# Kernel tuning notes

Measured on AMD Instinct MI355X. Metric: run time of the kernel, lower is better.

Reference implementation:

```python
import jax, jax.numpy as jnp
import numpy as np

N = 50000      # nodes
IN = 128       # in_channels
H = 2          # heads
C = 64         # hidden_channels (per head)
E = 800000     # edges (before self-loops)
OUT = 40       # out_channels
BN_EPS = 1e-5
NEG_SLOPE = 0.2  # PyG GATConv default


def _bn(x, g, b):
    # BatchNorm1d forward with batch statistics (training-mode math, biased var)
    mu = jnp.mean(x, axis=0)
    v = jnp.var(x, axis=0)
    return (x - mu) * jax.lax.rsqrt(v + BN_EPS) * g + b


def _gat_conv(x, src, dst, W, a_src, a_dst, bias, concat):
    n = x.shape[0]
    h = (x @ W).reshape(n, H, C)                      # [N,H,C] per-head projection
    al_s = jnp.einsum('nhc,hc->nh', h, a_src)         # [N,H]
    al_d = jnp.einsum('nhc,hc->nh', h, a_dst)
    e = jax.nn.leaky_relu(al_s[src] + al_d[dst], NEG_SLOPE)  # [E,H]
    # segment softmax over edges sharing the same destination
    m = jax.ops.segment_max(e, dst, num_segments=n)
    ex = jnp.exp(e - m[dst])
    s = jax.ops.segment_sum(ex, dst, num_segments=n)
    alpha = ex / s[dst]                               # [E,H]
    out = jax.ops.segment_sum(h[src] * alpha[..., None], dst, num_segments=n)  # [N,H,C]
    out = out.reshape(n, H * C) if concat else out.mean(axis=1)
    return out + bias


def setup_inputs() -> dict:
    key = jax.random.key(0)
    ks = jax.random.split(key, 16)
    g = lambda k, shp, scale=1.0: jax.random.normal(k, shp, dtype=jnp.float32) * scale
    x = g(ks[0], (N, IN))
    edge_index = jax.random.randint(ks[1], (2, E), 0, N, dtype=jnp.int32)
    s = 1.0 / np.sqrt(IN)
    s2 = 1.0 / np.sqrt(H * C)
    return {
        'x': x,
        'edge_index': edge_index,
        'bn0_g': jnp.ones((IN,), jnp.float32), 'bn0_b': jnp.zeros((IN,), jnp.float32),
        'W1': g(ks[2], (IN, H * C), s), 'a1_src': g(ks[3], (H, C), s), 'a1_dst': g(ks[4], (H, C), s),
        'b1': jnp.zeros((H * C,), jnp.float32),
        'bn1_g': jnp.ones((H * C,), jnp.float32), 'bn1_b': jnp.zeros((H * C,), jnp.float32),
        'W2': g(ks[5], (H * C, H * C), s2), 'a2_src': g(ks[6], (H, C), s2), 'a2_dst': g(ks[7], (H, C), s2),
        'b2': jnp.zeros((C,), jnp.float32),
        'bn2_g': jnp.ones((C,), jnp.float32), 'bn2_b': jnp.zeros((C,), jnp.float32),
        'Wf': g(ks[8], (C, OUT), 1.0 / np.sqrt(C)), 'bf': jnp.zeros((OUT,), jnp.float32),
    }


def reference(x, edge_index, bn0_g, bn0_b, W1, a1_src, a1_dst, b1, bn1_g, bn1_b,
              W2, a2_src, a2_dst, b2, bn2_g, bn2_b, Wf, bf):
    n = x.shape[0]
    loop = jnp.arange(n, dtype=edge_index.dtype)
    src = jnp.concatenate([edge_index[0], loop])  # add self-loops (PyG default)
    dst = jnp.concatenate([edge_index[1], loop])
    h = _bn(x, bn0_g, bn0_b)
    # layer 1: concat heads
    h = _gat_conv(h, src, dst, W1, a1_src, a1_dst, b1, concat=True)
    h = jax.nn.elu(_bn(h, bn1_g, bn1_b))
    # (dropout is identity in eval mode)
    # layer 2: average heads
    h = _gat_conv(h, src, dst, W2, a2_src, a2_dst, b2, concat=False)
    h = jax.nn.elu(_bn(h, bn2_g, bn2_b))
    return h @ Wf + bf
```

## Files before the change

kernel.cpp:

```cpp
#include <hip/hip_runtime.h>
#include <hip/hip_fp16.h>


#define NEG_SLOPE 0.2f
#define BN_EPS 1e-5f

typedef short bf16x8 __attribute__((ext_vector_type(8)));
typedef float f32x4 __attribute__((ext_vector_type(4)));

static __device__ __forceinline__ unsigned short f2bf(float f) {
    union { float f; unsigned u; } v; v.f = f;
    unsigned r = v.u + 0x7FFF + ((v.u >> 16) & 1);
    return (unsigned short)(r >> 16);
}
static __device__ __forceinline__ float2 bf2x2(unsigned v) {
    union { unsigned u; float f; } a, b;
    a.u = v << 16; b.u = v & 0xffff0000u;
    return make_float2(a.f, b.f);
}
static __device__ __forceinline__ float halfsel(unsigned p, int head) {
    __half2 h = *(__half2*)&p;
    return head ? __high2float(h) : __low2float(h);
}

template <int C>
static __device__ __forceinline__ void d_bnstat(const float* __restrict__ x, int M,
                                                int rowsPerBlock, float* __restrict__ sums,
                                                int b) {
    constexpr int TPR = C / 4;
    constexpr int RS  = 256 / TPR;
    __shared__ float red[4][2 * C];
    const int t = threadIdx.x;
    const int cg = t % TPR, rg = t / TPR, w = t >> 6, lane = t & 63;
    int r0 = b * rowsPerBlock + rg;
    int r1 = min(M, b * rowsPerBlock + rowsPerBlock);
    float4 s = make_float4(0, 0, 0, 0), q = make_float4(0, 0, 0, 0);
    #pragma unroll 4
    for (int r = r0; r < r1; r += RS) {
        float4 v = *(const float4*)&x[(size_t)r * C + cg * 4];
        s.x += v.x; s.y += v.y; s.z += v.z; s.w += v.w;
        q.x += v.x * v.x; q.y += v.y * v.y; q.z += v.z * v.z; q.w += v.w * v.w;
    }
    #pragma unroll
    for (int off = TPR; off < 64; off <<= 1) {
        s.x += __shfl_xor(s.x, off); s.y += __shfl_xor(s.y, off);
        s.z += __shfl_xor(s.z, off); s.w += __shfl_xor(s.w, off);
        q.x += __shfl_xor(q.x, off); q.y += __shfl_xor(q.y, off);
        q.z += __shfl_xor(q.z, off); q.w += __shfl_xor(q.w, off);
    }
    if (lane < TPR) {
        *(float4*)&red[w][cg * 4] = s;
        *(float4*)&red[w][C + cg * 4] = q;
    }
    __syncthreads();
    for (int idx = t; idx < 2 * C; idx += 256) {
        float tot = red[0][idx] + red[1][idx] + red[2][idx] + red[3][idx];
        atomicAdd(&sums[idx], tot);
    }
}

template <int C>
__global__ __launch_bounds__(256) void k_bnstat2(const float* __restrict__ x, int M,
                                                 int rowsPerBlock, float* __restrict__ sums) {
    d_bnstat<C>(x, M, rowsPerBlock, sums, blockIdx.x);
}

__global__ __launch_bounds__(256) void k_prep(
    const int* __restrict__ ei, int E, int rgrid,
    const float* __restrict__ x, int M, int bgrid,
    const float* __restrict__ W1, const float* __restrict__ W2,
    int* __restrict__ cnt, unsigned short* __restrict__ rank,
    float* __restrict__ sums,
    unsigned short* __restrict__ wt1, unsigned short* __restrict__ wt2) {
    int b = blockIdx.x;
    if (b < rgrid) {
        int i = b * 256 + threadIdx.x;
        if (i < E) {
            int d = ei[E + i];
            int p = b & 7;
            rank[i] = (unsigned short)atomicAdd(&cnt[(size_t)p * M + d], 1);
        }
    } else if (b < rgrid + bgrid) {
        d_bnstat<128>(x, M, 256, sums, b - rgrid);
    } else {
        int idx = (b - rgrid - bgrid) * 256 + threadIdx.x;
        if (idx < 128 * 128) {
            int n = idx >> 7, k = idx & 127;
            wt1[idx] = f2bf(W1[k * 128 + n]);
            wt2[idx] = f2bf(W2[k * 128 + n]);
        }
    }
}

__global__ __launch_bounds__(1024) void k_part(const int* __restrict__ cnt, int Nn,
                                               int* __restrict__ part) {
    __shared__ int ws[16];
    int t = threadIdx.x, lane = t & 63, w = t >> 6;
    int i = blockIdx.x * 1024 + t;
    int v = 0;
    if (i < Nn) {
        #pragma unroll
        for (int p = 0; p < 8; p++) v += cnt[(size_t)p * Nn + i];
        v += 1;
    }
    #pragma unroll
    for (int off = 32; off; off >>= 1) v += __shfl_xor(v, off);
    if (lane == 0) ws[w] = v;
    __syncthreads();
    if (t < 16) {
        int s = ws[t];
        #pragma unroll
        for (int off = 8; off; off >>= 1) s += __shfl_xor(s, off);
        if (t == 0) part[blockIdx.x] = s;
    }
}

__global__ __launch_bounds__(1024) void k_scan2(const int* __restrict__ cnt, int Nn, int nb,
                                                const int* __restrict__ part,
                                                int* __restrict__ rowptr,
                                                unsigned short* __restrict__ pofs) {
    __shared__ int wsum[16];
    __shared__ int s_base, s_total;
    int t = threadIdx.x, lane = t & 63, w = t >> 6;
    int b = blockIdx.x;
    if (w == 0) {
        int base = 0, total = 0;
        for (int ch = 0; ch < nb; ch += 64) {
            int j = ch + lane;
            int v = (j < nb) ? part[j] : 0;
            total += v;
            base += (j < b) ? v : 0;
        }
        #pragma unroll
        for (int off = 32; off; off >>= 1) {
            base += __shfl_xor(base, off);
            total += __shfl_xor(total, off);
        }
        if (lane == 0) { s_base = base; s_total = total; }
    }
    int i = b * 1024 + t;
    int v = 0;
    if (i < Nn) {
        int run = 0;
        #pragma unroll
        for (int p = 0; p < 8; p++) {
            pofs[(size_t)p * Nn + i] = (unsigned short)run;
            run += cnt[(size_t)p * Nn + i];
        }
        v = run + 1;
    }
    int x = v;
    #pragma unroll
    for (int off = 1; off < 64; off <<= 1) {
        int y = __shfl_up(x, off);
        if (lane >= off) x += y;
    }
    if (lane == 63) wsum[w] = x;
    __syncthreads();
    if (w == 0) {
        int val = (lane < 16) ? wsum[lane] : 0;
        int xs = val;
        #pragma unroll
        for (int off = 1; off < 16; off <<= 1) {
            int y = __shfl_up(xs, off);
            if (lane >= off) xs += y;
        }
        if (lane < 16) wsum[lane] = xs - val;
    }
    __syncthreads();
    if (i < Nn) rowptr[i] = s_base + wsum[w] + (x - v);
    if (b == nb - 1 && t == 0) rowptr[Nn] = s_total;
}

static __device__ __forceinline__ void d_fill(int b, const int* __restrict__ ei,
                                              const unsigned short* __restrict__ rank,
                                              const unsigned short* __restrict__ pofs,
                                              const int* __restrict__ rowptr, int E, int Nn,
                                              unsigned short* __restrict__ ssrc) {
    int i = b * 256 + threadIdx.x;
    if (i < E) {
        int s = ei[i], d = ei[E + i];
        int p = (i >> 8) & 7;
        int r = (int)pofs[(size_t)p * Nn + d] + (int)rank[i];
        ssrc[rowptr[d] + 1 + r] = (unsigned short)s;
    } else if (i < E + Nn) {
        int d = i - E;
        ssrc[rowptr[d]] = (unsigned short)d;
    }
}

static __device__ __forceinline__ void d_mfma(
    int blk, const float* __restrict__ A, const unsigned short* __restrict__ wt,
    const float* __restrict__ sums, const float* __restrict__ bng, const float* __restrict__ bnb,
    int elu, const float* __restrict__ asrc, const float* __restrict__ adst, int M,
    unsigned short* __restrict__ hb, float* __restrict__ als, float* __restrict__ ald) {
    __shared__ unsigned short As[64 * 136];
    __shared__ unsigned short Bs[128 * 136];
    __shared__ __align__(16) float stl[256];
    const int t = threadIdx.x;
    const int w = t >> 6, lane = t & 63;
    const int c = lane & 15, q = lane >> 4;
    const int row0 = blk * 64;

    if (t < 128) {
        float mu = sums[t] / (float)M;
        float var = sums[128 + t] / (float)M - mu * mu;
        float s = bng[t] * rsqrtf(var + BN_EPS);
        stl[t] = s;
        stl[128 + t] = bnb[t] - mu * s;
    }
    __syncthreads();

    #pragma unroll
    for (int i = 0; i < 8; i++) {
        int idx = t + i * 256;
        int r = idx >> 5, ch4 = idx & 31;
        int gr = row0 + r;
        float4 v = make_float4(0, 0, 0, 0);
        if (gr < M) {
            v = *(const float4*)&A[(size_t)gr * 128 + ch4 * 4];
            float4 sc = *(const float4*)&stl[ch4 * 4];
            float4 sh = *(const float4*)&stl[128 + ch4 * 4];
            v.x = v.x * sc.x + sh.x; v.y = v.y * sc.y + sh.y;
            v.z = v.z * sc.z + sh.z; v.w = v.w * sc.w + sh.w;
            if (elu) {
                v.x = v.x > 0.f ? v.x : expm1f(v.x);
                v.y = v.y > 0.f ? v.y : expm1f(v.y);
                v.z = v.z > 0.f ? v.z : expm1f(v.z);
                v.w = v.w > 0.f ? v.w : expm1f(v.w);
            }
        }
        unsigned p0 = ((unsigned)f2bf(v.y) << 16) | f2bf(v.x);
        unsigned p1 = ((unsigned)f2bf(v.w) << 16) | f2bf(v.z);
        *(uint2*)&As[r * 136 + ch4 * 4] = make_uint2(p0, p1);
    }
    #pragma unroll
    for (int i = 0; i < 8; i++) {
        int idx = t + i * 256;
        int r = idx >> 4, ch = idx & 15;
        *(uint4*)&Bs[r * 136 + ch * 8] = *(const uint4*)&wt[(size_t)r * 128 + ch * 8];
    }
    __syncthreads();

    f32x4 acc[8] = {};
    #pragma unroll
    for (int ks = 0; ks < 4; ks++) {
        bf16x8 a = *(bf16x8*)&As[(w * 16 + c) * 136 + (ks * 4 + q) * 8];
        #pragma unroll
        for (int tl = 0; tl < 8; tl++) {
            bf16x8 b = *(bf16x8*)&Bs[(tl * 16 + c) * 136 + (ks * 4 + q) * 8];
            acc[tl] = __builtin_amdgcn_mfma_f32_16x16x32_bf16(a, b, acc[tl], 0, 0, 0);
        }
    }

    #pragma unroll
    for (int reg = 0; reg < 4; reg++) {
        int grow = row0 + w * 16 + q * 4 + reg;
        if (grow < M) {
            #pragma unroll
            for (int tl = 0; tl < 8; tl++)
                hb[(size_t)grow * 128 + tl * 16 + c] = f2bf(acc[tl][reg]);
        }
    }

    float as_[8], ad_[8];
    #pragma unroll
    for (int tl = 0; tl < 8; tl++) { as_[tl] = asrc[tl * 16 + c]; ad_[tl] = adst[tl * 16 + c]; }
    #pragma unroll
    for (int reg = 0; reg < 4; reg++) {
        float s0 = 0.f, s1 = 0.f, d0 = 0.f, d1 = 0.f;
        #pragma unroll
        for (int tl = 0; tl < 4; tl++) { s0 += acc[tl][reg] * as_[tl]; d0 += acc[tl][reg] * ad_[tl]; }
        #pragma unroll
        for (int tl = 4; tl < 8; tl++) { s1 += acc[tl][reg] * as_[tl]; d1 += acc[tl][reg] * ad_[tl]; }
        #pragma unroll
        for (int off = 1; off < 16; off <<= 1) {
            s0 += __shfl_xor(s0, off); s1 += __shfl_xor(s1, off);
            d0 += __shfl_xor(d0, off); d1 += __shfl_xor(d1, off);
        }
        int grow = row0 + w * 16 + q * 4 + reg;
        if (c == 0 && grow < M) {
            *(float2*)&als[(size_t)grow * 2] = make_float2(s0, s1);
            *(float2*)&ald[(size_t)grow * 2] = make_float2(d0, d1);
        }
    }
}

__global__ __launch_bounds__(256) void k_mfma(
    const float* __restrict__ A, const unsigned short* __restrict__ wt,
    const float* __restrict__ sums, const float* __restrict__ bng, const float* __restrict__ bnb,
    int elu, const float* __restrict__ asrc, const float* __restrict__ adst, int M,
    unsigned short* __restrict__ hb, float* __restrict__ als, float* __restrict__ ald) {
    d_mfma(blockIdx.x, A, wt, sums, bng, bnb, elu, asrc, adst, M, hb, als, ald);
}

__global__ __launch_bounds__(256) void k_fill_mfma(
    const float* __restrict__ A, const unsigned short* __restrict__ wt,
    const float* __restrict__ sums, const float* __restrict__ bng, const float* __restrict__ bnb,
    const float* __restrict__ asrc, const float* __restrict__ adst, int M, int ggrid,
    unsigned short* __restrict__ hb, float* __restrict__ als, float* __restrict__ ald,
    const int* __restrict__ ei, const unsigned short* __restrict__ rank,
    const unsigned short* __restrict__ pofs,
    const int* __restrict__ rowptr, int E, int Nn, unsigned short* __restrict__ ssrc) {
    if (blockIdx.x < ggrid)
        d_mfma(blockIdx.x, A, wt, sums, bng, bnb, 0, asrc, adst, M, hb, als, ald);
    else
        d_fill(blockIdx.x - ggrid, ei, rank, pofs, rowptr, E, Nn, ssrc);
}

static __device__ __forceinline__ void acc8(float* acc, uint4 v, float a) {
    float2 p;
    p = bf2x2(v.x); acc[0] += a * p.x; acc[1] += a * p.y;
    p = bf2x2(v.y); acc[2] += a * p.x; acc[3] += a * p.y;
    p = bf2x2(v.z); acc[4] += a * p.x; acc[5] += a * p.y;
    p = bf2x2(v.w); acc[6] += a * p.x; acc[7] += a * p.y;
}

template <int MEAN>
static __device__ __forceinline__ void attnagg(
    const int* __restrict__ rowptr, const unsigned short* __restrict__ ssrc,
    const float* __restrict__ als, const float* __restrict__ ald,
    float* __restrict__ alpha, const unsigned short* __restrict__ hb,
    const float* __restrict__ bias, int Nn, float* __restrict__ out) {
    int gw = (blockIdx.x * blockDim.x + threadIdx.x) >> 6;
    if (gw >= Nn) return;
    int lane = threadIdx.x & 63;
    int sub = lane >> 4, c = lane & 15, head = c >> 3;
    int beg = rowptr[gw], end = rowptr[gw + 1];
    int deg = end - beg;
    float2 dv = *(const float2*)&ald[(size_t)gw * 2];
    float acc[8] = {};

    if (deg <= 64) {
        bool on = lane < deg;
        int eidx = beg + (on ? lane : 0);
        int sreg = (int)ssrc[eidx];
        float2 av = *(const float2*)&als[(size_t)sreg * 2];
        float v0 = av.x + dv.x; v0 = v0 > 0.f ? v0 : NEG_SLOPE * v0;
        float v1 = av.y + dv.y; v1 = v1 > 0.f ? v1 : NEG_SLOPE * v1;
        float p0 = on ? __expf(v0) : 0.f;
        float p1 = on ? __expf(v1) : 0.f;
        float t0 = p0, t1 = p1;
        #pragma unroll
        for (int off = 32; off; off >>= 1) {
            t0 += __shfl_xor(t0, off);
            t1 += __shfl_xor(t1, off);
        }
        __half2 hpk = __floats2half2_rn(p0 / t0, p1 / t1);
        unsigned pk = *(unsigned*)&hpk;

        int nit = (deg + 3) >> 2;
        int it = 0;
        for (; it + 4 <= nit; it += 4) {
            int s_[4]; float a_[4];
            #pragma unroll
            for (int u = 0; u < 4; u++) {
                int jj = (it + u) * 4 + sub;
                int ls = jj & 63;
                s_[u] = __shfl(sreg, ls);
                unsigned pw = (unsigned)__shfl(pk, ls);
                a_[u] = (jj < deg) ? halfsel(pw, head) : 0.f;
            }
            #pragma unroll
            for (int u = 0; u < 4; u++) {
                uint4 v = *(const uint4*)&hb[(size_t)s_[u] * 128 + c * 8];
                acc8(acc, v, a_[u]);
            }
        }
        for (; it < nit; it += 2) {
            const bool two = (it + 1) < nit;
            int s_[2]; float a_[2];
            #pragma unroll
            for (int u = 0; u < 2; u++) {
                if (u == 0 || two) {
                    int jj = (it + u) * 4 + sub;
                    int ls = jj & 63;
                    s_[u] = __shfl(sreg, ls);
                    unsigned pw = (unsigned)__shfl(pk, ls);
                    a_[u] = (jj < deg) ? halfsel(pw, head) : 0.f;
                }
            }
            #pragma unroll
            for (int u = 0; u < 2; u++) {
                if (u == 0 || two) {
                    uint4 v = *(const uint4*)&hb[(size_t)s_[u] * 128 + c * 8];
                    acc8(acc, v, a_[u]);
                }
            }
        }
    } else {
        float d0 = dv.x, d1 = dv.y;
        float m0 = -1e30f, m1 = -1e30f;
        for (int e = beg + lane; e < end; e += 64) {
            int s = (int)ssrc[e];
            float v0 = als[s * 2] + d0;     v0 = v0 > 0.f ? v0 : NEG_SLOPE * v0;
            float v1 = als[s * 2 + 1] + d1; v1 = v1 > 0.f ? v1 : NEG_SLOPE * v1;
            m0 = fmaxf(m0, v0); m1 = fmaxf(m1, v1);
        }
        #pragma unroll
        for (int off = 32; off; off >>= 1) {
            m0 = fmaxf(m0, __shfl_xor(m0, off));
            m1 = fmaxf(m1, __shfl_xor(m1, off));
        }
        float t0 = 0.f, t1 = 0.f;
        for (int e = beg + lane; e < end; e += 64) {
            int s = (int)ssrc[e];
            float v0 = als[s * 2] + d0;     v0 = v0 > 0.f ? v0 : NEG_SLOPE * v0;
            float v1 = als[s * 2 + 1] + d1; v1 = v1 > 0.f ? v1 : NEG_SLOPE * v1;
            float p0 = __expf(v0 - m0), p1 = __expf(v1 - m1);
            alpha[e * 2] = p0; alpha[e * 2 + 1] = p1;
            t0 += p0; t1 += p1;
        }
        #pragma unroll
        for (int off = 32; off; off >>= 1) {
            t0 += __shfl_xor(t0, off);
            t1 += __shfl_xor(t1, off);
        }
        float i0 = 1.f / t0, i1 = 1.f / t1;
        for (int e = beg + sub; e < end; e += 4) {
            int s = (int)ssrc[e];
            float a = (head ? alpha[(size_t)e * 2 + 1] * i1 : alpha[(size_t)e * 2] * i0);
            uint4 v = *(const uint4*)&hb[(size_t)s * 128 + c * 8];
            acc8(acc, v, a);
        }
    }

    #pragma unroll
    for (int j2 = 0; j2 < 8; j2++) {
        acc[j2] += __shfl_xor(acc[j2], 16);
        acc[j2] += __shfl_xor(acc[j2], 32);
        if (MEAN) acc[j2] += __shfl_xor(acc[j2], 8);
    }
    if (MEAN) {
        if (sub == 0 && c < 8) {
            float4 b0 = *(const float4*)&bias[c * 8];
            float4 b1 = *(const float4*)&bias[c * 8 + 4];
            float4 o0 = make_float4(0.5f * acc[0] + b0.x, 0.5f * acc[1] + b0.y, 0.5f * acc[2] + b0.z, 0.5f * acc[3] + b0.w);
            float4 o1 = make_float4(0.5f * acc[4] + b1.x, 0.5f * acc[5] + b1.y, 0.5f * acc[6] + b1.z, 0.5f * acc[7] + b1.w);
            *(float4*)&out[(size_t)gw * 64 + c * 8] = o0;
            *(float4*)&out[(size_t)gw * 64 + c * 8 + 4] = o1;
        }
    } else {
        if (sub == 0) {
            float4 b0 = *(const float4*)&bias[c * 8];
            float4 b1 = *(const float4*)&bias[c * 8 + 4];
            float4 o0 = make_float4(acc[0] + b0.x, acc[1] + b0.y, acc[2] + b0.z, acc[3] + b0.w);
            float4 o1 = make_float4(acc[4] + b1.x, acc[5] + b1.y, acc[6] + b1.z, acc[7] + b1.w);
            *(float4*)&out[(size_t)gw * 128 + c * 8] = o0;
            *(float4*)&out[(size_t)gw * 128 + c * 8 + 4] = o1;
        }
    }
}

__global__ __launch_bounds__(256) void k_attnagg1(const int* __restrict__ rowptr, const unsigned short* __restrict__ ssrc,
                                                  const float* __restrict__ als, const float* __restrict__ ald,
                                                  float* __restrict__ alpha, const unsigned short* __restrict__ hb,
                                                  const float* __restrict__ bias, int Nn, float* __restrict__ out) {
    attnagg<0>(rowptr, ssrc, als, ald, alpha, hb, bias, Nn, out);
}

__global__ __launch_bounds__(256) void k_attnagg2(const int* __restrict__ rowptr, const unsigned short* __restrict__ ssrc,
                                                  const float* __restrict__ als, const float* __restrict__ ald,
                                                  float* __restrict__ alpha, const unsigned short* __restrict__ hb,
                                                  const float* __restrict__ bias, int Nn, float* __restrict__ out) {
    attnagg<1>(rowptr, ssrc, als, ald, alpha, hb, bias, Nn, out);
}

__global__ __launch_bounds__(128) void k_gemmf(const float* __restrict__ A, const float* __restrict__ Wf,
                                               const float* __restrict__ bf,
                                               const float* __restrict__ sums, const float* __restrict__ bng,
                                               const float* __restrict__ bnb,
                                               int M, float* __restrict__ out) {
    __shared__ float As[128 * 65];
    __shared__ float Bs[64 * 40];
    __shared__ float stl[128];
    int t = threadIdx.x;
    int row0 = blockIdx.x * 128;
    if (t < 64) {
        float mu = sums[t] / (float)M;
        float var = sums[64 + t] / (float)M - mu * mu;
        float s = bng[t] * rsqrtf(var + BN_EPS);
        stl[t] = s;
        stl[64 + t] = bnb[t] - mu * s;
    }
    __syncthreads();
    for (int i = t; i < 64 * 40; i += 128) Bs[i] = Wf[i];
    for (int i = t; i < 128 * 64; i += 128) {
        int r = i >> 6, k = i & 63;
        int gr = row0 + r;
        float v = 0.f;
        if (gr < M) {
            v = A[(size_t)gr * 64 + k] * stl[k] + stl[64 + k];
            v = v > 0.f ? v : expm1f(v);
        }
        As[r * 65 + k] = v;
    }
    __syncthreads();
    int cg = t & 3, rg = t >> 2;
    float acc[4][10] = {};
    for (int k = 0; k < 64; k++) {
        float b[10];
        #pragma unroll
        for (int j = 0; j < 10; j++) b[j] = Bs[k * 40 + cg * 10 + j];
        #pragma unroll
        for (int r = 0; r < 4; r++) {
            float a = As[(rg * 4 + r) * 65 + k];
            #pragma unroll
            for (int j = 0; j < 10; j++) acc[r][j] += a * b[j];
        }
    }
    for (int r = 0; r < 4; r++) {
        int gr = row0 + rg * 4 + r;
        if (gr < M) {
            #pragma unroll
            for (int j = 0; j < 10; j++) out[(size_t)gr * 40 + cg * 10 + j] = acc[r][j] + bf[cg * 10 + j];
        }
    }
}

extern "C" void kernel_launch(void* const* d_in, const int* in_sizes, int n_in,
                              void* d_out, int out_size, void* d_ws, size_t ws_size,
                              hipStream_t stream) {
    const float* x     = (const float*)d_in[0];
    const int*   ei    = (const int*)d_in[1];
    const float* bn0_g = (const float*)d_in[2];
    const float* bn0_b = (const float*)d_in[3];
    const float* W1    = (const float*)d_in[4];
    const float* a1s   = (const float*)d_in[5];
    const float* a1d   = (const float*)d_in[6];
    const float* b1    = (const float*)d_in[7];
    const float* bn1_g = (const float*)d_in[8];
    const float* bn1_b = (const float*)d_in[9];
    const float* W2    = (const float*)d_in[10];
    const float* a2s   = (const float*)d_in[11];
    const float* a2d   = (const float*)d_in[12];
    const float* b2    = (const float*)d_in[13];
    const float* bn2_g = (const float*)d_in[14];
    const float* bn2_b = (const float*)d_in[15];
    const float* Wf    = (const float*)d_in[16];
    const float* bf    = (const float*)d_in[17];
    float* out = (float*)d_out;

    const int N  = in_sizes[0] / 128;
    const int E  = in_sizes[1] / 2;
    const int ET = E + N;

    char* ws = (char*)d_ws;
    size_t off = 0;
    auto alloc = [&](size_t bytes) -> char* {
        char* p = ws + off;
        off = (off + bytes + 255) & ~(size_t)255;
        return p;
    };
    int*   cnt    = (int*)alloc((size_t)8 * N * 4);
    float* sums   = (float*)alloc(640 * 4);
    const size_t zlen = off;
    int*   rowptr = (int*)alloc((size_t)(N + 1) * 4);
    unsigned short* ssrc = (unsigned short*)alloc((size_t)ET * 2);
    unsigned short* rank = (unsigned short*)alloc((size_t)E * 2);
    unsigned short* pofs = (unsigned short*)alloc((size_t)8 * N * 2);
    float* abuf   = (float*)alloc((size_t)N * 128 * 4);
    unsigned short* hb  = (unsigned short*)alloc((size_t)N * 128 * 2);
    unsigned short* wt1 = (unsigned short*)alloc((size_t)128 * 128 * 2);
    unsigned short* wt2 = (unsigned short*)alloc((size_t)128 * 128 * 2);
    float* alpha  = (float*)alloc((size_t)ET * 2 * 4);
    float* als    = (float*)alloc((size_t)N * 2 * 4);
    float* ald    = (float*)alloc((size_t)N * 2 * 4);
    int*   part   = (int*)alloc(1024 * 4);

    const int tb = 256;
    const int rgrid = (E + tb - 1) / tb;
    const int bgrid = (N + 255) / 256;
    const int fgrid = (ET + tb - 1) / tb;
    const int wgrid = ((size_t)N * 64 + tb - 1) / tb;
    const int ggrid = (N + 63) / 64;
    const int nscan = (N + 1023) / 1024;

    hipMemsetAsync(ws, 0, zlen, stream);

    k_prep<<<rgrid + bgrid + 64, tb, 0, stream>>>(ei, E, rgrid, x, N, bgrid, W1, W2,
                                                  cnt, rank, sums, wt1, wt2);
    k_part<<<nscan, 1024, 0, stream>>>(cnt, N, part);
    k_scan2<<<nscan, 1024, 0, stream>>>(cnt, N, nscan, part, rowptr, pofs);

    k_fill_mfma<<<ggrid + fgrid, tb, 0, stream>>>(x, wt1, sums, bn0_g, bn0_b,
                                                  a1s, a1d, N, ggrid, hb, als, ald,
                                                  ei, rank, pofs, rowptr, E, N, ssrc);
    k_attnagg1<<<wgrid, tb, 0, stream>>>(rowptr, ssrc, als, ald, alpha, hb, b1, N, abuf);

    k_bnstat2<128><<<bgrid, 256, 0, stream>>>(abuf, N, 256, sums + 256);

    k_mfma<<<ggrid, tb, 0, stream>>>(abuf, wt2, sums + 256, bn1_g, bn1_b, 1, a2s, a2d, N, hb, als, ald);
    k_attnagg2<<<wgrid, tb, 0, stream>>>(rowptr, ssrc, als, ald, alpha, hb, b2, N, abuf);

    k_bnstat2<64><<<bgrid, 256, 0, stream>>>(abuf, N, 256, sums + 512);

    k_gemmf<<<(N + 127) / 128, 128, 0, stream>>>(abuf, Wf, bf, sums + 512, bn2_g, bn2_b, N, out);
}
```

Baseline: 308.6 us.

## Count edge ranks with LDS histograms per node-range and edge-segment

Replaces the global-atomic degree counting, which used 8 partitioned int counters, with blocks that each own one edge segment of 32768 edges and one eighth of the node range. Each block histograms its destinations in shared memory, records ranks, and writes ushort counts per segment. The scan kernel turns these counts into per-segment offsets in place, so the separate pofs buffer and the zero-memset of cnt go away. In exchange, every block rereads its whole edge segment, so edge reads grow eightfold, and the scan kernels now loop over about 25 segments instead of 8.

```diff
diff --git a/kernel.cpp b/kernel.cpp
--- a/kernel.cpp
+++ b/kernel.cpp
@@ -66,24 +66,39 @@
 }
 
 __global__ __launch_bounds__(256) void k_prep(
-    const int* __restrict__ ei, int E, int rgrid,
+    const int* __restrict__ ei, int E, int S, int NR,
     const float* __restrict__ x, int M, int bgrid,
     const float* __restrict__ W1, const float* __restrict__ W2,
-    int* __restrict__ cnt, unsigned short* __restrict__ rank,
+    unsigned short* __restrict__ cnt, unsigned short* __restrict__ rank,
     float* __restrict__ sums,
     unsigned short* __restrict__ wt1, unsigned short* __restrict__ wt2) {
     int b = blockIdx.x;
-    if (b < rgrid) {
-        int i = b * 256 + threadIdx.x;
-        if (i < E) {
-            int d = ei[E + i];
-            int p = b & 7;
-            rank[i] = (unsigned short)atomicAdd(&cnt[(size_t)p * M + d], 1);
-        }
-    } else if (b < rgrid + bgrid) {
-        d_bnstat<128>(x, M, 256, sums, b - rgrid);
+    int CG = 8 * S;
+    if (b < CG) {
+        __shared__ unsigned lcnt[8192];
+        const int t = threadIdx.x;
+        const int r = b & 7, s = b >> 3;
+        const unsigned lo = (unsigned)(r * NR);
+        for (int j = t; j < NR; j += 256) lcnt[j] = 0;
+        __syncthreads();
+        int i1 = min(E, (s + 1) << 15);
+        for (int i = (s << 15) + t; i < i1; i += 256) {
+            unsigned d = (unsigned)ei[E + i];
+            unsigned rel = d - lo;
+            if (rel < (unsigned)NR) {
+                unsigned old = atomicAdd(&lcnt[rel], 1u);
+                rank[i] = (unsigned short)old;
+            }
+        }
+        __syncthreads();
+        for (int j = t; j < NR; j += 256) {
+            int node = (int)lo + j;
+            if (node < M) cnt[(size_t)s * M + node] = (unsigned short)lcnt[j];
+        }
+    } else if (b < CG + bgrid) {
+        d_bnstat<128>(x, M, 256, sums, b - CG);
     } else {
-        int idx = (b - rgrid - bgrid) * 256 + threadIdx.x;
+        int idx = (b - CG - bgrid) * 256 + threadIdx.x;
         if (idx < 128 * 128) {
             int n = idx >> 7, k = idx & 127;
             wt1[idx] = f2bf(W1[k * 128 + n]);
@@ -92,15 +107,14 @@
     }
 }
 
-__global__ __launch_bounds__(1024) void k_part(const int* __restrict__ cnt, int Nn,
-                                               int* __restrict__ part) {
+__global__ __launch_bounds__(1024) void k_part(const unsigned short* __restrict__ cnt,
+                                               int Nn, int S, int* __restrict__ part) {
     __shared__ int ws[16];
     int t = threadIdx.x, lane = t & 63, w = t >> 6;
     int i = blockIdx.x * 1024 + t;
     int v = 0;
     if (i < Nn) {
-        #pragma unroll
-        for (int p = 0; p < 8; p++) v += cnt[(size_t)p * Nn + i];
+        for (int s = 0; s < S; s++) v += (int)cnt[(size_t)s * Nn + i];
         v += 1;
     }
     #pragma unroll
@@ -115,10 +129,10 @@
     }
 }
 
-__global__ __launch_bounds__(1024) void k_scan2(const int* __restrict__ cnt, int Nn, int nb,
+__global__ __launch_bounds__(1024) void k_scan2(unsigned short* __restrict__ cnt,
+                                                int Nn, int S, int nb,
                                                 const int* __restrict__ part,
-                                                int* __restrict__ rowptr,
-                                                unsigned short* __restrict__ pofs) {
+                                                int* __restrict__ rowptr) {
     __shared__ int wsum[16];
     __shared__ int s_base, s_total;
     int t = threadIdx.x, lane = t & 63, w = t >> 6;
@@ -142,10 +156,10 @@
     int v = 0;
     if (i < Nn) {
         int run = 0;
-        #pragma unroll
-        for (int p = 0; p < 8; p++) {
-            pofs[(size_t)p * Nn + i] = (unsigned short)run;
-            run += cnt[(size_t)p * Nn + i];
+        for (int s = 0; s < S; s++) {
+            int cv = (int)cnt[(size_t)s * Nn + i];
+            cnt[(size_t)s * Nn + i] = (unsigned short)run;
+            run += cv;
         }
         v = run + 1;
     }
@@ -180,9 +194,9 @@
     int i = b * 256 + threadIdx.x;
     if (i < E) {
         int s = ei[i], d = ei[E + i];
-        int p = (i >> 8) & 7;
-        int r = (int)pofs[(size_t)p * Nn + d] + (int)rank[i];
-        ssrc[rowptr[d] + 1 + r] = (unsigned short)s;
+        int p = i >> 15;
+        int rk = (int)pofs[(size_t)p * Nn + d] + (int)rank[i];
+        ssrc[rowptr[d] + 1 + rk] = (unsigned short)s;
     } else if (i < E + Nn) {
         int d = i - E;
         ssrc[rowptr[d]] = (unsigned short)d;
@@ -544,6 +558,8 @@
     const int N  = in_sizes[0] / 128;
     const int E  = in_sizes[1] / 2;
     const int ET = E + N;
+    const int S  = (E + 32767) >> 15;
+    const int NR = (N + 7) / 8;
 
     char* ws = (char*)d_ws;
     size_t off = 0;
@@ -552,13 +568,12 @@
         off = (off + bytes + 255) & ~(size_t)255;
         return p;
     };
-    int*   cnt    = (int*)alloc((size_t)8 * N * 4);
     float* sums   = (float*)alloc(640 * 4);
     const size_t zlen = off;
+    unsigned short* cnt = (unsigned short*)alloc((size_t)S * N * 2);
     int*   rowptr = (int*)alloc((size_t)(N + 1) * 4);
     unsigned short* ssrc = (unsigned short*)alloc((size_t)ET * 2);
     unsigned short* rank = (unsigned short*)alloc((size_t)E * 2);
-    unsigned short* pofs = (unsigned short*)alloc((size_t)8 * N * 2);
     float* abuf   = (float*)alloc((size_t)N * 128 * 4);
     unsigned short* hb  = (unsigned short*)alloc((size_t)N * 128 * 2);
     unsigned short* wt1 = (unsigned short*)alloc((size_t)128 * 128 * 2);
@@ -569,7 +584,7 @@
     int*   part   = (int*)alloc(1024 * 4);
 
     const int tb = 256;
-    const int rgrid = (E + tb - 1) / tb;
+    const int CG = 8 * S;
     const int bgrid = (N + 255) / 256;
     const int fgrid = (ET + tb - 1) / tb;
     const int wgrid = ((size_t)N * 64 + tb - 1) / tb;
@@ -578,14 +593,14 @@
 
     hipMemsetAsync(ws, 0, zlen, stream);
 
-    k_prep<<<rgrid + bgrid + 64, tb, 0, stream>>>(ei, E, rgrid, x, N, bgrid, W1, W2,
-                                                  cnt, rank, sums, wt1, wt2);
-    k_part<<<nscan, 1024, 0, stream>>>(cnt, N, part);
-    k_scan2<<<nscan, 1024, 0, stream>>>(cnt, N, nscan, part, rowptr, pofs);
+    k_prep<<<CG + bgrid + 64, tb, 0, stream>>>(ei, E, S, NR, x, N, bgrid, W1, W2,
+                                               cnt, rank, sums, wt1, wt2);
+    k_part<<<nscan, 1024, 0, stream>>>(cnt, N, S, part);
+    k_scan2<<<nscan, 1024, 0, stream>>>(cnt, N, S, nscan, part, rowptr);
 
     k_fill_mfma<<<ggrid + fgrid, tb, 0, stream>>>(x, wt1, sums, bn0_g, bn0_b,
                                                   a1s, a1d, N, ggrid, hb, als, ald,
-                                                  ei, rank, pofs, rowptr, E, N, ssrc);
+                                                  ei, rank, cnt, rowptr, E, N, ssrc);
     k_attnagg1<<<wgrid, tb, 0, stream>>>(rowptr, ssrc, als, ald, alpha, hb, b1, N, abuf);
 
     k_bnstat2<128><<<bgrid, 256, 0, stream>>>(abuf, N, 256, sums + 256);
```

Result: slower. 330.4 us (+7.1%).
